# Performance work log

Hardware: AMD Instinct MI355X
Metric: run time of the kernel (lower is better)

## Reference

```python
import jax, jax.numpy as jnp
import numpy as np

MAX_WORDS = 256  # = batch['labels'].shape[1]


def _align(hidden, word_ids, max_words):
    """Batched segment-mean: (B,S,D) subtoken states -> (B,max_words,D) word states.
    Equivalent to align_subtokens_to_words applied per sample (word_ids all valid)."""
    B, S, D = hidden.shape
    seg = (word_ids.astype(jnp.int32) + jnp.arange(B, dtype=jnp.int32)[:, None] * max_words).reshape(-1)
    sums = jax.ops.segment_sum(hidden.reshape(-1, D), seg, num_segments=B * max_words)
    cnts = jax.ops.segment_sum(jnp.ones((B * S,), hidden.dtype), seg, num_segments=B * max_words)
    out = jnp.where(cnts[:, None] > 0, sums / jnp.maximum(cnts, 1.0)[:, None], 0.0)
    return out.reshape(B, max_words, D)


def setup_inputs() -> dict:
    key = jax.random.key(0)
    ks = jax.random.split(key, 8)
    B, S, D, W = 64, 512, 768, MAX_WORDS
    h_hing_sub = jax.random.normal(ks[0], (B, S, D), dtype=jnp.float32)
    h_rob_sub = jax.random.normal(ks[1], (B, S, D), dtype=jnp.float32)
    hing_word_ids = jnp.sort(jax.random.randint(ks[2], (B, S), 0, W), axis=-1).astype(jnp.int32)
    rob_word_ids = jnp.sort(jax.random.randint(ks[3], (B, S), 0, W), axis=-1).astype(jnp.int32)
    num_words = jax.random.randint(ks[4], (B,), 1, W).astype(jnp.int32)
    router_w1 = jax.random.normal(ks[5], (2 * D, 256), dtype=jnp.float32) * (1.0 / np.sqrt(2 * D))
    router_b1 = jnp.zeros((256,), jnp.float32)
    router_w2 = jax.random.normal(ks[6], (256, 1), dtype=jnp.float32) * (1.0 / 16.0)
    router_b2 = jnp.zeros((1,), jnp.float32)
    head_w = jax.random.normal(ks[7], (D, 7), dtype=jnp.float32) * (1.0 / np.sqrt(D))
    head_b = jnp.zeros((7,), jnp.float32)
    return {
        'h_hing_sub': h_hing_sub, 'h_rob_sub': h_rob_sub,
        'hing_word_ids': hing_word_ids, 'rob_word_ids': rob_word_ids,
        'num_words': num_words,
        'router_w1': router_w1, 'router_b1': router_b1,
        'router_w2': router_w2, 'router_b2': router_b2,
        'head_w': head_w, 'head_b': head_b,
    }


def reference(h_hing_sub, h_rob_sub, hing_word_ids, rob_word_ids, num_words,
              router_w1, router_b1, router_w2, router_b2, head_w, head_b):
    W = MAX_WORDS
    # scatter-mean subtokens -> words (the dominant custom-kernel op)
    h_hing = _align(h_hing_sub, hing_word_ids, W)   # (B, W, 768)
    h_rob = _align(h_rob_sub, rob_word_ids, W)      # (B, W, 768)
    # token-level MLP router on concatenated word states (router_input='both')
    router_in = jnp.concatenate([h_hing, h_rob], axis=-1)             # (B, W, 1536)
    hdn = jax.nn.relu(jnp.einsum('bwd,dh->bwh', router_in, router_w1) + router_b1)
    alpha = jax.nn.sigmoid(jnp.einsum('bwh,ho->bwo', hdn, router_w2) + router_b2)  # (B, W, 1)
    blended = alpha * h_hing + (1.0 - alpha) * h_rob                  # (B, W, 768)
    logits = jnp.einsum('bwd,dl->bwl', blended, head_w) + head_b      # (B, W, num_labels)
    l2_disagreement = jnp.linalg.norm(h_hing - h_rob, axis=-1)        # (B, W)
    return logits, alpha.squeeze(-1), l2_disagreement
```

## Files before the change

kernel.cpp:

```cpp
#include <hip/hip_runtime.h>
#include <hip/hip_bf16.h>
#include <math.h>

#define BATCH 64
#define SEQ   512
#define DIM   768
#define NW    256
#define NT    (BATCH * NW)
#define KDIM  1536
#define HID   256
#define NL    7

#define BM  32
#define BK  64
#define BKP 72
#define NKT (KDIM / BK)

#define WC  8

typedef __bf16 bf16_t;
typedef bf16_t bf16x4 __attribute__((ext_vector_type(4)));
typedef bf16_t bf16x8 __attribute__((ext_vector_type(8)));
typedef float  f32x4  __attribute__((ext_vector_type(4)));

__global__ __launch_bounds__(256) void convert_w1_kernel(
    const float* __restrict__ w1, bf16_t* __restrict__ w1t)
{
    int kc = blockIdx.x >> 3;
    int kg = blockIdx.x & 7;
    int n  = threadIdx.x;
    bf16x8 v;
    #pragma unroll
    for (int j = 0; j < 8; j++)
        v[j] = (bf16_t)w1[(size_t)(kc * 64 + kg * 8 + j) * HID + n];
    *(bf16x8*)(w1t + (size_t)kc * (HID * BK) + n * BK + kg * 8) = v;
}

__global__ __launch_bounds__(256) void starts_kernel(
    const int* __restrict__ idh, const int* __restrict__ idr,
    int* __restrict__ starts)
{
    int blk = blockIdx.x;
    int t = blk >> 6;
    int b = blk & 63;
    const int* ids = (t ? idr : idh) + b * SEQ;
    int w = threadIdx.x;
    int lo = 0, hi = SEQ;
    while (lo < hi) {
        int m = (lo + hi) >> 1;
        if (ids[m] < w) lo = m + 1; else hi = m;
    }
    int* row = starts + blk * 257;
    row[w] = lo;
    if (w == 0) row[256] = SEQ;
}

__global__ __launch_bounds__(256) void align_kernel(
    const float* __restrict__ hh, const float* __restrict__ hr,
    const int* __restrict__ starts, bf16_t* __restrict__ X)
{
    int tid  = threadIdx.x;
    int lane = tid & 63;
    int wv   = tid >> 6;
    int task = blockIdx.x * 4 + wv;
    int b = task >> 6;
    int t = (task >> 5) & 1;
    int c = task & 31;
    int w0 = c * WC;

    const int*   st    = starts + (t * 64 + b) * 257;
    const f32x4* base4 = (const f32x4*)((t ? hr : hh) + (size_t)b * SEQ * DIM);
    bf16_t*      dstb  = X + (size_t)b * NW * KDIM + t * DIM;

    int lo = st[w0];
    #pragma unroll 1
    for (int w = w0; w < w0 + WC; w++) {
        int hi = st[w + 1];
        bf16_t* xr = dstb + (size_t)w * KDIM;
        if (hi > lo) {
            f32x4 a0 = {0,0,0,0}, a1 = {0,0,0,0}, a2 = {0,0,0,0};
            for (int s = lo; s < hi; s++) {
                const f32x4* row = base4 + (size_t)s * (DIM / 4);
                a0 += row[lane];
                a1 += row[lane + 64];
                a2 += row[lane + 128];
            }
            float inv = 1.0f / (float)(hi - lo);
            bf16x4 o0, o1, o2;
            #pragma unroll
            for (int e = 0; e < 4; e++) {
                o0[e] = (bf16_t)(a0[e] * inv);
                o1[e] = (bf16_t)(a1[e] * inv);
                o2[e] = (bf16_t)(a2[e] * inv);
            }
            *(bf16x4*)(xr + (lane)       * 4) = o0;
            *(bf16x4*)(xr + (lane + 64)  * 4) = o1;
            *(bf16x4*)(xr + (lane + 128) * 4) = o2;
        } else {
            bf16x4 z = {};
            *(bf16x4*)(xr + (lane)       * 4) = z;
            *(bf16x4*)(xr + (lane + 64)  * 4) = z;
            *(bf16x4*)(xr + (lane + 128) * 4) = z;
        }
        lo = hi;
    }
}

__global__ __launch_bounds__(256) void gemm_alpha_kernel(
    const bf16_t* __restrict__ X, const bf16_t* __restrict__ w1t,
    const float* __restrict__ b1, const float* __restrict__ w2,
    const float* __restrict__ b2, float* __restrict__ out)
{
    __shared__ __align__(16) bf16_t Xs[BM][BKP];
    __shared__ __align__(16) bf16_t Ws[HID][BKP];
    __shared__ float alpha_acc[BM];

    int tid   = threadIdx.x;
    int lane  = tid & 63;
    int wv    = tid >> 6;
    int row16 = lane & 15;
    int quad  = lane >> 4;
    int tok0  = blockIdx.x * BM;

    f32x4 acc[2][4];
    #pragma unroll
    for (int mi = 0; mi < 2; mi++)
        #pragma unroll
        for (int ni = 0; ni < 4; ni++)
            acc[mi][ni] = (f32x4){0.f, 0.f, 0.f, 0.f};

    int xr = tid >> 3;
    int xc = tid & 7;

    for (int kc = 0; kc < NKT; kc++) {
        {
            const uint4* src = (const uint4*)(X + (size_t)(tok0 + xr) * KDIM + kc * BK + xc * 8);
            *(uint4*)(&Xs[xr][xc * 8]) = *src;
        }
        {
            const uint4* srcb = (const uint4*)(w1t + (size_t)kc * (HID * BK));
            #pragma unroll
            for (int i = 0; i < 8; i++) {
                int cidx = tid + i * 256;
                *(uint4*)(&Ws[cidx >> 3][(cidx & 7) * 8]) = srcb[cidx];
            }
        }
        __syncthreads();
        #pragma unroll
        for (int kk2 = 0; kk2 < 2; kk2++) {
            bf16x8 af[2], bfg[4];
            #pragma unroll
            for (int mi = 0; mi < 2; mi++)
                af[mi] = *(const bf16x8*)(&Xs[mi * 16 + row16][kk2 * 32 + quad * 8]);
            #pragma unroll
            for (int ni = 0; ni < 4; ni++)
                bfg[ni] = *(const bf16x8*)(&Ws[wv * 64 + ni * 16 + row16][kk2 * 32 + quad * 8]);
            #pragma unroll
            for (int mi = 0; mi < 2; mi++)
                #pragma unroll
                for (int ni = 0; ni < 4; ni++)
                    acc[mi][ni] = __builtin_amdgcn_mfma_f32_16x16x32_bf16(
                        af[mi], bfg[ni], acc[mi][ni], 0, 0, 0);
        }
        __syncthreads();
    }

    float w2v[4], b1v[4];
    #pragma unroll
    for (int ni = 0; ni < 4; ni++) {
        int col = wv * 64 + ni * 16 + row16;
        w2v[ni] = w2[col];
        b1v[ni] = b1[col];
    }
    if (tid < BM) alpha_acc[tid] = 0.f;
    __syncthreads();

    #pragma unroll
    for (int mi = 0; mi < 2; mi++) {
        #pragma unroll
        for (int r = 0; r < 4; r++) {
            float p = 0.f;
            #pragma unroll
            for (int ni = 0; ni < 4; ni++) {
                float v = acc[mi][ni][r] + b1v[ni];
                v = v > 0.f ? v : 0.f;
                p += v * w2v[ni];
            }
            p += __shfl_xor(p, 1);
            p += __shfl_xor(p, 2);
            p += __shfl_xor(p, 4);
            p += __shfl_xor(p, 8);
            if (row16 == 0)
                atomicAdd(&alpha_acc[mi * 16 + quad * 4 + r], p);
        }
    }
    __syncthreads();
    if (tid < BM) {
        float a = 1.f / (1.f + expf(-(alpha_acc[tid] + b2[0])));
        out[(size_t)NT * NL + tok0 + tid] = a;
    }
}

__global__ __launch_bounds__(256) void blend_kernel(
    const bf16_t* __restrict__ X, const float* __restrict__ hw,
    const float* __restrict__ hb, float* __restrict__ out)
{
    __shared__ float hws[NL * DIM];
    int tid  = threadIdx.x;
    int lane = tid & 63;
    int wv   = tid >> 6;

    for (int i = tid; i < DIM * NL; i += 256) {
        int d = i / NL, l = i - d * NL;
        hws[l * DIM + d] = hw[i];
    }
    __syncthreads();

    int tok = blockIdx.x * 4 + wv;
    const float* alpha = out + (size_t)NT * NL;
    float a = alpha[tok];
    const bf16_t* xrow = X + (size_t)tok * KDIM;

    float lg[NL] = {0.f, 0.f, 0.f, 0.f, 0.f, 0.f, 0.f};
    float l2 = 0.f;

    #pragma unroll
    for (int j = 0; j < 3; j++) {
        int d0 = (lane + 64 * j) * 4;
        bf16x4 hp = *(const bf16x4*)(xrow + d0);
        bf16x4 rp = *(const bf16x4*)(xrow + DIM + d0);
        float bl[4];
        #pragma unroll
        for (int e = 0; e < 4; e++) {
            float hhv = (float)hp[e];
            float hrv = (float)rp[e];
            bl[e] = a * hhv + (1.f - a) * hrv;
            float df = hhv - hrv;
            l2 += df * df;
        }
        #pragma unroll
        for (int l = 0; l < NL; l++) {
            f32x4 wv4 = *(const f32x4*)(&hws[l * DIM + d0]);
            lg[l] += bl[0] * wv4[0] + bl[1] * wv4[1] + bl[2] * wv4[2] + bl[3] * wv4[3];
        }
    }

    #pragma unroll
    for (int off = 1; off < 64; off <<= 1) {
        #pragma unroll
        for (int l = 0; l < NL; l++) lg[l] += __shfl_xor(lg[l], off);
        l2 += __shfl_xor(l2, off);
    }

    if (lane < NL)
        out[(size_t)tok * NL + lane] = lg[lane] + hb[lane];
    else if (lane == NL)
        out[(size_t)NT * NL + NT + tok] = sqrtf(l2);
}

extern "C" void kernel_launch(void* const* d_in, const int* in_sizes, int n_in,
                              void* d_out, int out_size, void* d_ws, size_t ws_size,
                              hipStream_t stream)
{
    const float* hh  = (const float*)d_in[0];
    const float* hr  = (const float*)d_in[1];
    const int*   idh = (const int*)d_in[2];
    const int*   idr = (const int*)d_in[3];
    const float* w1  = (const float*)d_in[5];
    const float* b1  = (const float*)d_in[6];
    const float* w2  = (const float*)d_in[7];
    const float* b2  = (const float*)d_in[8];
    const float* hw  = (const float*)d_in[9];
    const float* hb  = (const float*)d_in[10];
    float* out = (float*)d_out;

    bf16_t* X      = (bf16_t*)d_ws;
    bf16_t* w1t    = X + (size_t)NT * KDIM;
    int*    starts = (int*)(w1t + (size_t)NKT * HID * BK);

    convert_w1_kernel<<<192, 256, 0, stream>>>(w1, w1t);
    starts_kernel<<<128, 256, 0, stream>>>(idh, idr, starts);
    align_kernel<<<1024, 256, 0, stream>>>(hh, hr, starts, X);
    gemm_alpha_kernel<<<NT / BM, 256, 0, stream>>>(X, w1t, b1, w2, b2, out);
    blend_kernel<<<NT / 4, 256, 0, stream>>>(X, hw, hb, out);
}
```

Before: 305.1 us.

## Restructure align, GEMM, blend and weight conversion kernels for memory-level parallelism

The align kernel now runs half as many words per wave over twice as many blocks, and it issues up to six row loads up front so more memory requests are in flight. The GEMM drops shared-memory staging and reads MFMA fragments straight from global memory through a row-major transposed W1, which also removes the per-tile syncs. The blend kernel packs 8 tokens per wave, uses wider bf16x8 loads and a shorter shuffle reduction, which amortises the per-block shared-memory load of head weights. Weight conversion uses an LDS transpose tile. The direct global loads in the GEMM rely on cache hits and may lose the reuse that the LDS staging gave.

```diff
diff --git a/kernel.cpp b/kernel.cpp
--- a/kernel.cpp
+++ b/kernel.cpp
@@ -11,13 +11,6 @@
 #define HID   256
 #define NL    7
 
-#define BM  32
-#define BK  64
-#define BKP 72
-#define NKT (KDIM / BK)
-
-#define WC  8
-
 typedef __bf16 bf16_t;
 typedef bf16_t bf16x4 __attribute__((ext_vector_type(4)));
 typedef bf16_t bf16x8 __attribute__((ext_vector_type(8)));
@@ -26,14 +19,23 @@
 __global__ __launch_bounds__(256) void convert_w1_kernel(
     const float* __restrict__ w1, bf16_t* __restrict__ w1t)
 {
-    int kc = blockIdx.x >> 3;
-    int kg = blockIdx.x & 7;
-    int n  = threadIdx.x;
-    bf16x8 v;
-    #pragma unroll
-    for (int j = 0; j < 8; j++)
-        v[j] = (bf16_t)w1[(size_t)(kc * 64 + kg * 8 + j) * HID + n];
-    *(bf16x8*)(w1t + (size_t)kc * (HID * BK) + n * BK + kg * 8) = v;
+    __shared__ float tile[32 * 257];
+    int tid = threadIdx.x;
+    int k0  = blockIdx.x * 32;
+
+    for (int kk = 0; kk < 32; kk++)
+        tile[kk * 257 + tid] = w1[(size_t)(k0 + kk) * HID + tid];
+    __syncthreads();
+
+    int n = tid;
+    #pragma unroll
+    for (int c = 0; c < 4; c++) {
+        bf16x8 v;
+        #pragma unroll
+        for (int j = 0; j < 8; j++)
+            v[j] = (bf16_t)tile[(c * 8 + j) * 257 + n];
+        *(bf16x8*)(w1t + (size_t)n * KDIM + k0 + c * 8) = v;
+    }
 }
 
 __global__ __launch_bounds__(256) void starts_kernel(
@@ -63,10 +65,10 @@
     int lane = tid & 63;
     int wv   = tid >> 6;
     int task = blockIdx.x * 4 + wv;
-    int b = task >> 6;
-    int t = (task >> 5) & 1;
-    int c = task & 31;
-    int w0 = c * WC;
+    int b = task >> 7;
+    int t = (task >> 6) & 1;
+    int c = task & 63;
+    int w0 = c * 4;
 
     const int*   st    = starts + (t * 64 + b) * 257;
     const f32x4* base4 = (const f32x4*)((t ? hr : hh) + (size_t)b * SEQ * DIM);
@@ -74,18 +76,41 @@
 
     int lo = st[w0];
     #pragma unroll 1
-    for (int w = w0; w < w0 + WC; w++) {
+    for (int w = w0; w < w0 + 4; w++) {
         int hi = st[w + 1];
+        int n  = hi - lo;
+        int ns = __builtin_amdgcn_readfirstlane(n);
         bf16_t* xr = dstb + (size_t)w * KDIM;
-        if (hi > lo) {
-            f32x4 a0 = {0,0,0,0}, a1 = {0,0,0,0}, a2 = {0,0,0,0};
-            for (int s = lo; s < hi; s++) {
-                const f32x4* row = base4 + (size_t)s * (DIM / 4);
-                a0 += row[lane];
-                a1 += row[lane + 64];
-                a2 += row[lane + 128];
+
+        if (ns <= 0) {
+            bf16x4 z = {};
+            *(bf16x4*)(xr + lane * 4)         = z;
+            *(bf16x4*)(xr + (lane + 64) * 4)  = z;
+            *(bf16x4*)(xr + (lane + 128) * 4) = z;
+        } else {
+            const f32x4* r0 = base4 + (size_t)lo * (DIM / 4);
+            f32x4 z = {0.f, 0.f, 0.f, 0.f};
+            f32x4 l0a=z,l0b=z,l0c=z, l1a=z,l1b=z,l1c=z, l2a=z,l2b=z,l2c=z;
+            f32x4 l3a=z,l3b=z,l3c=z, l4a=z,l4b=z,l4c=z, l5a=z,l5b=z,l5c=z;
+            {                 l0a=r0[lane]; l0b=r0[lane+64]; l0c=r0[lane+128]; }
+            if (ns > 1) { const f32x4* r=r0+192;   l1a=r[lane]; l1b=r[lane+64]; l1c=r[lane+128]; }
+            if (ns > 2) { const f32x4* r=r0+384;   l2a=r[lane]; l2b=r[lane+64]; l2c=r[lane+128]; }
+            if (ns > 3) { const f32x4* r=r0+576;   l3a=r[lane]; l3b=r[lane+64]; l3c=r[lane+128]; }
+            if (ns > 4) { const f32x4* r=r0+768;   l4a=r[lane]; l4b=r[lane+64]; l4c=r[lane+128]; }
+            if (ns > 5) { const f32x4* r=r0+960;   l5a=r[lane]; l5b=r[lane+64]; l5c=r[lane+128]; }
+
+            f32x4 a0 = z, a1 = z, a2 = z;
+            if (ns > 6) {
+                for (int s = lo + 6; s < hi; s++) {
+                    const f32x4* r = base4 + (size_t)s * (DIM / 4);
+                    a0 += r[lane]; a1 += r[lane + 64]; a2 += r[lane + 128];
+                }
             }
-            float inv = 1.0f / (float)(hi - lo);
+            a0 += (l0a + l1a) + (l2a + l3a) + (l4a + l5a);
+            a1 += (l0b + l1b) + (l2b + l3b) + (l4b + l5b);
+            a2 += (l0c + l1c) + (l2c + l3c) + (l4c + l5c);
+
+            float inv = 1.0f / (float)n;
             bf16x4 o0, o1, o2;
             #pragma unroll
             for (int e = 0; e < 4; e++) {
@@ -93,14 +118,9 @@
                 o1[e] = (bf16_t)(a1[e] * inv);
                 o2[e] = (bf16_t)(a2[e] * inv);
             }
-            *(bf16x4*)(xr + (lane)       * 4) = o0;
-            *(bf16x4*)(xr + (lane + 64)  * 4) = o1;
+            *(bf16x4*)(xr + lane * 4)         = o0;
+            *(bf16x4*)(xr + (lane + 64) * 4)  = o1;
             *(bf16x4*)(xr + (lane + 128) * 4) = o2;
-        } else {
-            bf16x4 z = {};
-            *(bf16x4*)(xr + (lane)       * 4) = z;
-            *(bf16x4*)(xr + (lane + 64)  * 4) = z;
-            *(bf16x4*)(xr + (lane + 128) * 4) = z;
         }
         lo = hi;
     }
@@ -111,16 +131,14 @@
     const float* __restrict__ b1, const float* __restrict__ w2,
     const float* __restrict__ b2, float* __restrict__ out)
 {
-    __shared__ __align__(16) bf16_t Xs[BM][BKP];
-    __shared__ __align__(16) bf16_t Ws[HID][BKP];
-    __shared__ float alpha_acc[BM];
+    __shared__ float alpha_acc[32];
 
     int tid   = threadIdx.x;
     int lane  = tid & 63;
     int wv    = tid >> 6;
     int row16 = lane & 15;
     int quad  = lane >> 4;
-    int tok0  = blockIdx.x * BM;
+    int tok0  = blockIdx.x * 32;
 
     f32x4 acc[2][4];
     #pragma unroll
@@ -129,40 +147,24 @@
         for (int ni = 0; ni < 4; ni++)
             acc[mi][ni] = (f32x4){0.f, 0.f, 0.f, 0.f};
 
-    int xr = tid >> 3;
-    int xc = tid & 7;
-
-    for (int kc = 0; kc < NKT; kc++) {
-        {
-            const uint4* src = (const uint4*)(X + (size_t)(tok0 + xr) * KDIM + kc * BK + xc * 8);
-            *(uint4*)(&Xs[xr][xc * 8]) = *src;
-        }
-        {
-            const uint4* srcb = (const uint4*)(w1t + (size_t)kc * (HID * BK));
-            #pragma unroll
-            for (int i = 0; i < 8; i++) {
-                int cidx = tid + i * 256;
-                *(uint4*)(&Ws[cidx >> 3][(cidx & 7) * 8]) = srcb[cidx];
-            }
-        }
-        __syncthreads();
-        #pragma unroll
-        for (int kk2 = 0; kk2 < 2; kk2++) {
-            bf16x8 af[2], bfg[4];
-            #pragma unroll
-            for (int mi = 0; mi < 2; mi++)
-                af[mi] = *(const bf16x8*)(&Xs[mi * 16 + row16][kk2 * 32 + quad * 8]);
+    const bf16_t* aptr = X   + (size_t)(tok0 + row16) * KDIM + quad * 8;
+    const bf16_t* bptr = w1t + (size_t)(wv * 64 + row16) * KDIM + quad * 8;
+
+    #pragma unroll 4
+    for (int kcc = 0; kcc < KDIM / 32; kcc++) {
+        bf16x8 af[2], bfg[4];
+        #pragma unroll
+        for (int mi = 0; mi < 2; mi++)
+            af[mi] = *(const bf16x8*)(aptr + (size_t)mi * 16 * KDIM + kcc * 32);
+        #pragma unroll
+        for (int ni = 0; ni < 4; ni++)
+            bfg[ni] = *(const bf16x8*)(bptr + (size_t)ni * 16 * KDIM + kcc * 32);
+        #pragma unroll
+        for (int mi = 0; mi < 2; mi++)
             #pragma unroll
             for (int ni = 0; ni < 4; ni++)
-                bfg[ni] = *(const bf16x8*)(&Ws[wv * 64 + ni * 16 + row16][kk2 * 32 + quad * 8]);
-            #pragma unroll
-            for (int mi = 0; mi < 2; mi++)
-                #pragma unroll
-                for (int ni = 0; ni < 4; ni++)
-                    acc[mi][ni] = __builtin_amdgcn_mfma_f32_16x16x32_bf16(
-                        af[mi], bfg[ni], acc[mi][ni], 0, 0, 0);
-        }
-        __syncthreads();
+                acc[mi][ni] = __builtin_amdgcn_mfma_f32_16x16x32_bf16(
+                    af[mi], bfg[ni], acc[mi][ni], 0, 0, 0);
     }
 
     float w2v[4], b1v[4];
@@ -172,7 +174,7 @@
         w2v[ni] = w2[col];
         b1v[ni] = b1[col];
     }
-    if (tid < BM) alpha_acc[tid] = 0.f;
+    if (tid < 32) alpha_acc[tid] = 0.f;
     __syncthreads();
 
     #pragma unroll
@@ -195,7 +197,7 @@
         }
     }
     __syncthreads();
-    if (tid < BM) {
+    if (tid < 32) {
         float a = 1.f / (1.f + expf(-(alpha_acc[tid] + b2[0])));
         out[(size_t)NT * NL + tok0 + tid] = a;
     }
@@ -216,46 +218,53 @@
     }
     __syncthreads();
 
-    int tok = blockIdx.x * 4 + wv;
-    const float* alpha = out + (size_t)NT * NL;
-    float a = alpha[tok];
+    int g   = lane >> 3;
+    int u   = lane & 7;
+    int tok = blockIdx.x * 32 + wv * 8 + g;
+
+    float a = out[(size_t)NT * NL + tok];
     const bf16_t* xrow = X + (size_t)tok * KDIM;
 
     float lg[NL] = {0.f, 0.f, 0.f, 0.f, 0.f, 0.f, 0.f};
     float l2 = 0.f;
 
     #pragma unroll
-    for (int j = 0; j < 3; j++) {
-        int d0 = (lane + 64 * j) * 4;
-        bf16x4 hp = *(const bf16x4*)(xrow + d0);
-        bf16x4 rp = *(const bf16x4*)(xrow + DIM + d0);
-        float bl[4];
-        #pragma unroll
-        for (int e = 0; e < 4; e++) {
+    for (int k = 0; k < 12; k++) {
+        int d0 = (k * 8 + u) * 8;
+        bf16x8 hp = *(const bf16x8*)(xrow + d0);
+        bf16x8 rp = *(const bf16x8*)(xrow + DIM + d0);
+        float bl[8];
+        #pragma unroll
+        for (int e = 0; e < 8; e++) {
             float hhv = (float)hp[e];
             float hrv = (float)rp[e];
-            bl[e] = a * hhv + (1.f - a) * hrv;
-            float df = hhv - hrv;
-            l2 += df * df;
+            float df  = hhv - hrv;
+            bl[e] = fmaf(a, df, hrv);
+            l2 = fmaf(df, df, l2);
         }
         #pragma unroll
         for (int l = 0; l < NL; l++) {
-            f32x4 wv4 = *(const f32x4*)(&hws[l * DIM + d0]);
-            lg[l] += bl[0] * wv4[0] + bl[1] * wv4[1] + bl[2] * wv4[2] + bl[3] * wv4[3];
-        }
-    }
-
-    #pragma unroll
-    for (int off = 1; off < 64; off <<= 1) {
+            f32x4 wA = *(const f32x4*)(&hws[l * DIM + d0]);
+            f32x4 wB = *(const f32x4*)(&hws[l * DIM + d0 + 4]);
+            lg[l] += bl[0]*wA[0] + bl[1]*wA[1] + bl[2]*wA[2] + bl[3]*wA[3]
+                   + bl[4]*wB[0] + bl[5]*wB[1] + bl[6]*wB[2] + bl[7]*wB[3];
+        }
+    }
+
+    #pragma unroll
+    for (int off = 1; off < 8; off <<= 1) {
         #pragma unroll
         for (int l = 0; l < NL; l++) lg[l] += __shfl_xor(lg[l], off);
         l2 += __shfl_xor(l2, off);
     }
 
-    if (lane < NL)
-        out[(size_t)tok * NL + lane] = lg[lane] + hb[lane];
-    else if (lane == NL)
+    if (u < NL) {
+        float v = (u == 0) ? lg[0] : (u == 1) ? lg[1] : (u == 2) ? lg[2]
+                : (u == 3) ? lg[3] : (u == 4) ? lg[4] : (u == 5) ? lg[5] : lg[6];
+        out[(size_t)tok * NL + u] = v + hb[u];
+    } else {
         out[(size_t)NT * NL + NT + tok] = sqrtf(l2);
+    }
 }
 
 extern "C" void kernel_launch(void* const* d_in, const int* in_sizes, int n_in,
@@ -276,11 +285,11 @@
 
     bf16_t* X      = (bf16_t*)d_ws;
     bf16_t* w1t    = X + (size_t)NT * KDIM;
-    int*    starts = (int*)(w1t + (size_t)NKT * HID * BK);
-
-    convert_w1_kernel<<<192, 256, 0, stream>>>(w1, w1t);
+    int*    starts = (int*)(w1t + (size_t)HID * KDIM);
+
+    convert_w1_kernel<<<48, 256, 0, stream>>>(w1, w1t);
     starts_kernel<<<128, 256, 0, stream>>>(idh, idr, starts);
-    align_kernel<<<1024, 256, 0, stream>>>(hh, hr, starts, X);
-    gemm_alpha_kernel<<<NT / BM, 256, 0, stream>>>(X, w1t, b1, w2, b2, out);
-    blend_kernel<<<NT / 4, 256, 0, stream>>>(X, hw, hb, out);
-}
+    align_kernel<<<2048, 256, 0, stream>>>(hh, hr, starts, X);
+    gemm_alpha_kernel<<<512, 256, 0, stream>>>(X, w1t, b1, w2, b2, out);
+    blend_kernel<<<512, 256, 0, stream>>>(X, hw, hb, out);
+}
```

Result: slower. 327.1 us (+7.2%).
